# Kernel optimization log

Hardware: AMD Instinct MI355X
Metric: run time of the kernel (lower is better)

## Reference

```python
import jax, jax.numpy as jnp
import numpy as np

NEG_INF = -1e8  # matches neg_inf in the numba kernel


def setup_inputs() -> dict:
    key = jax.random.key(0)
    k1, k2 = jax.random.split(key)
    B, N, M, S = 128, 256, 256, 3
    theta = jax.random.normal(k1, (B, N, M, S), dtype=jnp.float32)
    A = jax.random.normal(k2, (B, N, M, S, S), dtype=jnp.float32)
    # state transition offsets: match, insert, delete
    pos = jnp.array([[-1, -1], [-1, 0], [0, -1]], dtype=jnp.int64)
    return {"theta": theta, "A": A, "pos": pos}


def _forward(theta, A, pos):
    # theta: [B,N,M,S], A: [B,N,M,S,S], pos: [S,2] with entries in {(-1,-1),(-1,0),(0,-1)}
    B, N, M, S = theta.shape
    # map each state k to its source cell: 0 -> V[i-1,j-1], 1 -> V[i-1,j], 2 -> V[i,j-1]
    idx = jnp.where(pos[:, 0] == -1,
                    jnp.where(pos[:, 1] == -1, 0, 1), 2)  # [S]

    # v_prev holds row i-1, columns 0..M. Row 0: V[0,0,:]=0, rest = NEG_INF.
    v0 = jnp.full((B, M + 1, S), NEG_INF, theta.dtype)
    v0 = v0.at[:, 0, :].set(0.0)

    def row_step(v_prev, row):
        theta_r, A_r = row                               # [M,B,S], [M,B,S,S]
        prev_jm1 = jnp.swapaxes(v_prev[:, :M], 0, 1)     # V[i-1, j-1] : [M,B,S]
        prev_j = jnp.swapaxes(v_prev[:, 1:], 0, 1)       # V[i-1, j]   : [M,B,S]

        def col_step(v_left, xs):
            pjm1, pj, th, a = xs                         # [B,S],[B,S],[B,S],[B,S,S]
            cand = jnp.stack([pjm1, pj, v_left], axis=0) # [3,B,S]
            src = cand[idx]                              # [S,B,S]: source V per state k
            scores = jnp.swapaxes(src, 0, 1) + a         # [B,S(k),S(L)]
            v_new = jax.nn.logsumexp(scores, axis=-1) + th  # [B,S]
            return v_new, v_new

        v_left0 = jnp.full((B, S), NEG_INF, theta.dtype)  # column 0 boundary
        _, v_row = jax.lax.scan(col_step, v_left0, (prev_jm1, prev_j, theta_r, A_r))
        v_row = jnp.swapaxes(v_row, 0, 1)                # [B,M,S]
        v_prev_new = jnp.concatenate(
            [jnp.full((B, 1, S), NEG_INF, theta.dtype), v_row], axis=1)
        return v_prev_new, None

    theta_t = jnp.transpose(theta, (1, 2, 0, 3))  # [N,M,B,S]
    A_t = jnp.transpose(A, (1, 2, 0, 3, 4))       # [N,M,B,S,S]
    v_last, _ = jax.lax.scan(row_step, v0, (theta_t, A_t))
    # terminal log-partition: logsumexp over states at cell (N, M)
    return jax.nn.logsumexp(v_last[:, M, :], axis=-1)  # [B]


def reference(theta, A, pos):
    return _forward(theta, A, pos)
```

## Files before the change

### kernel.cpp

```cpp
#include <hip/hip_runtime.h>


#define NEG_INF -1.0e8f

constexpr int Nr = 256;
constexpr int Mc = 256;

typedef float v4f __attribute__((ext_vector_type(4)));

__device__ __forceinline__ float lae2(float x, float y) {
    float m = fmaxf(x, y);
    float d = fminf(x, y) - m;
    return m + __logf(1.0f + __expf(d));
}

__device__ __forceinline__ float lse3(float x0, float x1, float x2) {
    float m = fmaxf(x0, fmaxf(x1, x2));
    return m + __logf(__expf(x0 - m) + __expf(x1 - m) + __expf(x2 - m));
}

template <int CTRL>
__device__ __forceinline__ float dppf(float x) {
    int xi = __builtin_bit_cast(int, x);
    int ri = __builtin_amdgcn_update_dpp(xi, xi, CTRL, 0xF, 0xF, false);
    return __builtin_bit_cast(float, ri);
}

struct RowRegs { v4f t0, t1, t2, a0, a1, a2, a3, a4, a5, a6, a7, a8; };

#define GLOAD(dst, ptr, OFF)                                              \
    asm volatile("global_load_dwordx4 %0, %1, off offset:" #OFF          \
                 : "=v"(dst) : "v"(ptr))

#define ISSUE_ROW(S, tp, apn) do {                                        \
    GLOAD((S).t0, (tp), 0);   GLOAD((S).t1, (tp), 16);                    \
    GLOAD((S).t2, (tp), 32);                                              \
    GLOAD((S).a0, (apn), 0);  GLOAD((S).a1, (apn), 16);                   \
    GLOAD((S).a2, (apn), 32); GLOAD((S).a3, (apn), 48);                   \
    GLOAD((S).a4, (apn), 64); GLOAD((S).a5, (apn), 80);                   \
    GLOAD((S).a6, (apn), 96); GLOAD((S).a7, (apn), 112);                  \
    GLOAD((S).a8, (apn), 128);                                            \
} while (0)

#define WAITV(N) asm volatile("s_waitcnt vmcnt(" #N ")" ::: "memory")

#define UNPACK4(arr, off, v) do {                                         \
    arr[(off)+0] = (v)[0]; arr[(off)+1] = (v)[1];                         \
    arr[(off)+2] = (v)[2]; arr[(off)+3] = (v)[3]; } while (0)

#define ROW_STEP(rr, S_CUR, S_DST)                                        \
    WAITV(12);                                                            \
    __builtin_amdgcn_sched_barrier(0);                                    \
    ISSUE_ROW(S_DST, tN, aN); tN += Mc * 3; aN += Mc * 9;                 \
    __builtin_amdgcn_sched_barrier(0);                                    \
    compute_row((rr), S_CUR)

__global__ __launch_bounds__(64, 1)
void ForwardDecoder_kernel(const float* __restrict__ theta,
                           const float* __restrict__ A,
                           float* __restrict__ out) {
    const int b = blockIdx.x;
    const int L = threadIdx.x;

    const float* thp = theta + ((size_t)b * Nr * Mc + 4 * L) * 3;
    const float* ap  = A     + ((size_t)b * Nr * Mc + 4 * L) * 9;

    float pv0[4], pv1[4], pv2[4];
    #pragma unroll
    for (int j = 0; j < 4; ++j) { pv0[j] = NEG_INF; pv1[j] = NEG_INF; pv2[j] = NEG_INF; }

    auto compute_row = [&](int r, const RowRegs& S) {
        float Th[12], Aa[36];
        UNPACK4(Th, 0, S.t0);  UNPACK4(Th, 4, S.t1);  UNPACK4(Th, 8, S.t2);
        UNPACK4(Aa, 0, S.a0);  UNPACK4(Aa, 4, S.a1);  UNPACK4(Aa, 8, S.a2);
        UNPACK4(Aa,12, S.a3);  UNPACK4(Aa,16, S.a4);  UNPACK4(Aa,20, S.a5);
        UNPACK4(Aa,24, S.a6);  UNPACK4(Aa,28, S.a7);  UNPACK4(Aa,32, S.a8);

        float bl0 = dppf<0x138>(pv0[3]);
        float bl1 = dppf<0x138>(pv1[3]);
        float bl2 = dppf<0x138>(pv2[3]);
        if (L == 0) {
            float bv = (r == 0) ? 0.0f : NEG_INF;
            bl0 = bv; bl1 = bv; bl2 = bv;
        }

        float v0[4], v1[4];
        #pragma unroll
        for (int j = 0; j < 4; ++j) {
            float d0 = (j == 0) ? bl0 : pv0[j-1];
            float d1 = (j == 0) ? bl1 : pv1[j-1];
            float d2 = (j == 0) ? bl2 : pv2[j-1];
            const float* aj = &Aa[9*j];
            v0[j] = Th[3*j+0] + lse3(d0 + aj[0], d1 + aj[1], d2 + aj[2]);
            v1[j] = Th[3*j+1] + lse3(pv0[j] + aj[3], pv1[j] + aj[4], pv2[j] + aj[5]);
        }

        float lx0 = dppf<0x138>(v0[3]);
        float lx1 = dppf<0x138>(v1[3]);

        float pa[4], pb[4];
        #pragma unroll
        for (int j = 0; j < 4; ++j) {
            float n0 = (j == 0) ? lx0 : v0[j-1];
            float n1 = (j == 0) ? lx1 : v1[j-1];
            if (L == 0 && j == 0) { n0 = NEG_INF; n1 = NEG_INF; }
            const float* aj = &Aa[9*j];
            float a  = Th[3*j+2] + aj[8];
            float bb = Th[3*j+2] + lae2(n0 + aj[6], n1 + aj[7]);
            if (j == 0) { pa[0] = a; pb[0] = bb; }
            else        { pa[j] = pa[j-1] + a; pb[j] = lae2(a + pb[j-1], bb); }
        }

        float SA = pa[3], SB = pb[3];
        const int l16 = L & 15;
        { float ao = dppf<0x111>(SA), bo = dppf<0x111>(SB);
          if (l16 >= 1) { SB = lae2(SA + bo, SB); SA += ao; } }
        { float ao = dppf<0x112>(SA), bo = dppf<0x112>(SB);
          if (l16 >= 2) { SB = lae2(SA + bo, SB); SA += ao; } }
        { float ao = dppf<0x114>(SA), bo = dppf<0x114>(SB);
          if (l16 >= 4) { SB = lae2(SA + bo, SB); SA += ao; } }
        { float ao = dppf<0x118>(SA), bo = dppf<0x118>(SB);
          if (l16 >= 8) { SB = lae2(SA + bo, SB); SA += ao; } }
        { float ao = dppf<0x142>(SA), bo = dppf<0x142>(SB);
          if (L & 16)  { SB = lae2(SA + bo, SB); SA += ao; } }
        { float ao = dppf<0x143>(SA), bo = dppf<0x143>(SB);
          if (L >= 32) { SB = lae2(SA + bo, SB); SA += ao; } }

        float eA = dppf<0x138>(SA);
        float eB = dppf<0x138>(SB);
        float xL = (L == 0) ? NEG_INF : lae2(eA + NEG_INF, eB);

        float v2[4];
        #pragma unroll
        for (int j = 0; j < 4; ++j) v2[j] = lae2(pa[j] + xL, pb[j]);

        #pragma unroll
        for (int j = 0; j < 4; ++j) { pv0[j] = v0[j]; pv1[j] = v1[j]; pv2[j] = v2[j]; }

        if (r == Nr - 1 && L == 63) {
            out[b] = lse3(v0[3], v1[3], v2[3]);
        }
    };

    RowRegs S0, S1, S2, S3;
    const float* tN = thp;
    const float* aN = ap;

    ISSUE_ROW(S0, tN, aN); tN += Mc * 3; aN += Mc * 9;
    ISSUE_ROW(S1, tN, aN); tN += Mc * 3; aN += Mc * 9;

    for (int r = 0; r < Nr - 4; r += 4) {
        ROW_STEP(r + 0, S0, S2);
        ROW_STEP(r + 1, S1, S3);
        ROW_STEP(r + 2, S2, S0);
        ROW_STEP(r + 3, S3, S1);
    }

    WAITV(12); __builtin_amdgcn_sched_barrier(0);
    ISSUE_ROW(S2, tN, aN); tN += Mc * 3; aN += Mc * 9;
    __builtin_amdgcn_sched_barrier(0);
    compute_row(Nr - 4, S0);

    WAITV(12); __builtin_amdgcn_sched_barrier(0);
    ISSUE_ROW(S3, tN, aN);
    __builtin_amdgcn_sched_barrier(0);
    compute_row(Nr - 3, S1);

    WAITV(12); __builtin_amdgcn_sched_barrier(0);
    compute_row(Nr - 2, S2);

    WAITV(0);  __builtin_amdgcn_sched_barrier(0);
    compute_row(Nr - 1, S3);
}

extern "C" void kernel_launch(void* const* d_in, const int* in_sizes, int n_in,
                              void* d_out, int out_size, void* d_ws, size_t ws_size,
                              hipStream_t stream) {
    const float* theta = (const float*)d_in[0];
    const float* A     = (const float*)d_in[1];
    float* out = (float*)d_out;

    const int B = in_sizes[0] / (Nr * Mc * 3);
    ForwardDecoder_kernel<<<B, 64, 0, stream>>>(theta, A, out);
}
```

Before: 708.7 us.

## Warp-specialize loaders that stream rows into an LDS ring via global_load_lds

Adds four producer waves per block that prefetch each row's theta and A tiles two rows ahead into a four-slot LDS ring using direct global-to-LDS loads. The single compute wave then reads its per-row operands from LDS instead of holding them in registers from inline-asm global loads. This is meant to free compute-wave registers and keep memory traffic off the critical dependency chain. In exchange it adds a block-wide barrier on every row, and loads can become effectively synchronous per row if the barrier waits on outstanding memory operations.

```diff
diff --git a/kernel.cpp b/kernel.cpp
--- a/kernel.cpp
+++ b/kernel.cpp
@@ -5,8 +5,8 @@
 
 constexpr int Nr = 256;
 constexpr int Mc = 256;
-
-typedef float v4f __attribute__((ext_vector_type(4)));
+constexpr int NS = 4;
+constexpr int SLOT_F = 12 * 256;
 
 __device__ __forceinline__ float lae2(float x, float y) {
     float m = fmaxf(x, y);
@@ -26,55 +26,56 @@
     return __builtin_bit_cast(float, ri);
 }
 
-struct RowRegs { v4f t0, t1, t2, a0, a1, a2, a3, a4, a5, a6, a7, a8; };
-
-#define GLOAD(dst, ptr, OFF)                                              \
-    asm volatile("global_load_dwordx4 %0, %1, off offset:" #OFF          \
-                 : "=v"(dst) : "v"(ptr))
-
-#define ISSUE_ROW(S, tp, apn) do {                                        \
-    GLOAD((S).t0, (tp), 0);   GLOAD((S).t1, (tp), 16);                    \
-    GLOAD((S).t2, (tp), 32);                                              \
-    GLOAD((S).a0, (apn), 0);  GLOAD((S).a1, (apn), 16);                   \
-    GLOAD((S).a2, (apn), 32); GLOAD((S).a3, (apn), 48);                   \
-    GLOAD((S).a4, (apn), 64); GLOAD((S).a5, (apn), 80);                   \
-    GLOAD((S).a6, (apn), 96); GLOAD((S).a7, (apn), 112);                  \
-    GLOAD((S).a8, (apn), 128);                                            \
-} while (0)
-
-#define WAITV(N) asm volatile("s_waitcnt vmcnt(" #N ")" ::: "memory")
+__device__ __forceinline__ void gl_lds16(const void* g, void* l) {
+    __builtin_amdgcn_global_load_lds(
+        (const __attribute__((address_space(1))) void*)g,
+        (__attribute__((address_space(3))) void*)l,
+        16, 0, 0);
+}
 
 #define UNPACK4(arr, off, v) do {                                         \
-    arr[(off)+0] = (v)[0]; arr[(off)+1] = (v)[1];                         \
-    arr[(off)+2] = (v)[2]; arr[(off)+3] = (v)[3]; } while (0)
+    arr[(off)+0] = (v).x; arr[(off)+1] = (v).y;                           \
+    arr[(off)+2] = (v).z; arr[(off)+3] = (v).w; } while (0)
 
-#define ROW_STEP(rr, S_CUR, S_DST)                                        \
-    WAITV(12);                                                            \
-    __builtin_amdgcn_sched_barrier(0);                                    \
-    ISSUE_ROW(S_DST, tN, aN); tN += Mc * 3; aN += Mc * 9;                 \
-    __builtin_amdgcn_sched_barrier(0);                                    \
-    compute_row((rr), S_CUR)
-
-__global__ __launch_bounds__(64, 1)
+__global__ __launch_bounds__(320, 1)
 void ForwardDecoder_kernel(const float* __restrict__ theta,
                            const float* __restrict__ A,
                            float* __restrict__ out) {
-    const int b = blockIdx.x;
-    const int L = threadIdx.x;
+    __shared__ float lds[NS][SLOT_F];
 
-    const float* thp = theta + ((size_t)b * Nr * Mc + 4 * L) * 3;
-    const float* ap  = A     + ((size_t)b * Nr * Mc + 4 * L) * 9;
+    const int b    = blockIdx.x;
+    const int tid  = threadIdx.x;
+    const int wave = tid >> 6;
+    const int L    = tid & 63;
+
+    const char* thB = (const char*)theta + (size_t)b * Nr * Mc * 12;
+    const char* aB  = (const char*)A     + (size_t)b * Nr * Mc * 36;
+
+    auto issue_row = [&](int rn) {
+        const int slot = rn & (NS - 1);
+        const char* tr = thB + (size_t)rn * (Mc * 12) + 48 * L;
+        const char* ar = aB  + (size_t)rn * (Mc * 36) + 144 * L;
+        float* dst = &lds[slot][0];
+        gl_lds16(tr +  0, dst + 0 * 256);
+        gl_lds16(tr + 16, dst + 1 * 256);
+        gl_lds16(tr + 32, dst + 2 * 256);
+        #pragma unroll
+        for (int q = 0; q < 9; ++q)
+            gl_lds16(ar + 16 * q, dst + (3 + q) * 256);
+    };
 
     float pv0[4], pv1[4], pv2[4];
     #pragma unroll
     for (int j = 0; j < 4; ++j) { pv0[j] = NEG_INF; pv1[j] = NEG_INF; pv2[j] = NEG_INF; }
 
-    auto compute_row = [&](int r, const RowRegs& S) {
+    auto compute_row = [&](int r) {
+        const int slot = r & (NS - 1);
         float Th[12], Aa[36];
-        UNPACK4(Th, 0, S.t0);  UNPACK4(Th, 4, S.t1);  UNPACK4(Th, 8, S.t2);
-        UNPACK4(Aa, 0, S.a0);  UNPACK4(Aa, 4, S.a1);  UNPACK4(Aa, 8, S.a2);
-        UNPACK4(Aa,12, S.a3);  UNPACK4(Aa,16, S.a4);  UNPACK4(Aa,20, S.a5);
-        UNPACK4(Aa,24, S.a6);  UNPACK4(Aa,28, S.a7);  UNPACK4(Aa,32, S.a8);
+        const float4* c = reinterpret_cast<const float4*>(&lds[slot][0]);
+        #pragma unroll
+        for (int q = 0; q < 3; ++q) { float4 v = c[q * 64 + L]; UNPACK4(Th, 4 * q, v); }
+        #pragma unroll
+        for (int q = 0; q < 9; ++q) { float4 v = c[(3 + q) * 64 + L]; UNPACK4(Aa, 4 * q, v); }
 
         float bl0 = dppf<0x138>(pv0[3]);
         float bl1 = dppf<0x138>(pv1[3]);
@@ -142,35 +143,22 @@
         }
     };
 
-    RowRegs S0, S1, S2, S3;
-    const float* tN = thp;
-    const float* aN = ap;
+    if (wave > 0) {
+        const int lw = wave - 1;
+        if (lw == 0) issue_row(0);
+        if (lw == 1) issue_row(1);
+    }
+    __syncthreads();
 
-    ISSUE_ROW(S0, tN, aN); tN += Mc * 3; aN += Mc * 9;
-    ISSUE_ROW(S1, tN, aN); tN += Mc * 3; aN += Mc * 9;
-
-    for (int r = 0; r < Nr - 4; r += 4) {
-        ROW_STEP(r + 0, S0, S2);
-        ROW_STEP(r + 1, S1, S3);
-        ROW_STEP(r + 2, S2, S0);
-        ROW_STEP(r + 3, S3, S1);
+    for (int r = 0; r < Nr; ++r) {
+        if (wave == 0) {
+            compute_row(r);
+        } else {
+            const int rn = r + 2;
+            if (rn < Nr && (rn & 3) == (wave - 1)) issue_row(rn);
+        }
+        __syncthreads();
     }
-
-    WAITV(12); __builtin_amdgcn_sched_barrier(0);
-    ISSUE_ROW(S2, tN, aN); tN += Mc * 3; aN += Mc * 9;
-    __builtin_amdgcn_sched_barrier(0);
-    compute_row(Nr - 4, S0);
-
-    WAITV(12); __builtin_amdgcn_sched_barrier(0);
-    ISSUE_ROW(S3, tN, aN);
-    __builtin_amdgcn_sched_barrier(0);
-    compute_row(Nr - 3, S1);
-
-    WAITV(12); __builtin_amdgcn_sched_barrier(0);
-    compute_row(Nr - 2, S2);
-
-    WAITV(0);  __builtin_amdgcn_sched_barrier(0);
-    compute_row(Nr - 1, S3);
 }
 
 extern "C" void kernel_launch(void* const* d_in, const int* in_sizes, int n_in,
@@ -181,5 +169,5 @@
     float* out = (float*)d_out;
 
     const int B = in_sizes[0] / (Nr * Mc * 3);
-    ForwardDecoder_kernel<<<B, 64, 0, stream>>>(theta, A, out);
+    ForwardDecoder_kernel<<<B, 320, 0, stream>>>(theta, A, out);
 }
```

Result: slower. 731.4 us (+3.2%).
